# Optimization experiments

Measured on AMD Instinct MI355X. Metric: run time of the kernel, lower is better.

## Reference

```python
import jax, jax.numpy as jnp
import numpy as np

NUM_HEADS = 4
NUM_GROUPS = 32
EPS = 1e-5


def setup_inputs() -> dict:
    key = jax.random.key(0)
    ks = jax.random.split(key, 4)
    ch = 256
    x = jax.random.normal(ks[0], (16, ch, 32, 32), dtype=jnp.float32)
    gn_w = jnp.ones((ch,), jnp.float32)
    gn_b = jnp.zeros((ch,), jnp.float32)
    # conv1x1 weights, kaiming-ish scale
    qkv_w = jax.random.normal(ks[1], (3 * ch, ch), dtype=jnp.float32) / np.sqrt(ch)
    qkv_b = jnp.zeros((3 * ch,), jnp.float32)
    proj_w = jax.random.normal(ks[2], (ch, ch), dtype=jnp.float32) / np.sqrt(ch)
    proj_b = jnp.zeros((ch,), jnp.float32)
    return {"x": x, "gn_w": gn_w, "gn_b": gn_b, "qkv_w": qkv_w,
            "qkv_b": qkv_b, "proj_w": proj_w, "proj_b": proj_b}


def _group_norm(x, w, b):
    bsz, c, h, wd = x.shape
    g = NUM_GROUPS
    xg = x.reshape(bsz, g, c // g, h, wd)
    mean = xg.mean(axis=(2, 3, 4), keepdims=True)
    var = xg.var(axis=(2, 3, 4), keepdims=True)
    xg = (xg - mean) * jax.lax.rsqrt(var + EPS)
    return xg.reshape(bsz, c, h, wd) * w[None, :, None, None] + b[None, :, None, None]


def reference(x, gn_w, gn_b, qkv_w, qkv_b, proj_w, proj_b):
    b, c, h, w = x.shape
    hd = c // NUM_HEADS
    scale = hd ** (-0.5)
    y = _group_norm(x, gn_w, gn_b)
    # 1x1 conv == channel matmul
    qkv = jnp.einsum('oc,bchw->bohw', qkv_w, y) + qkv_b[None, :, None, None]
    q, k, v = jnp.split(qkv, 3, axis=1)
    q = q.reshape(b, NUM_HEADS, hd, h * w)
    k = k.reshape(b, NUM_HEADS, hd, h * w)
    v = v.reshape(b, NUM_HEADS, hd, h * w)
    attn = jnp.einsum('bhdi,bhdj->bhij', q * scale, k)
    attn = jax.nn.softmax(attn, axis=-1)
    out = jnp.einsum('bhij,bhdj->bhdi', attn, v)
    out = out.reshape(b, c, h, w)
    out = jnp.einsum('oc,bchw->bohw', proj_w, out) + proj_b[None, :, None, None]
    return x + out
```

## Files before the change

### kernel.cpp

```cpp
#include <hip/hip_runtime.h>
#include <cstddef>

#define B_   16
#define C_   256
#define HW_  1024
#define NH_  4
#define NG_  32
#define CPG_ 8

typedef __attribute__((ext_vector_type(8))) short bf16x8;
typedef __attribute__((ext_vector_type(8))) _Float16 f16x8;
typedef __attribute__((ext_vector_type(4))) float f32x4;

#define MFMA16B(a, b, c) __builtin_amdgcn_mfma_f32_16x16x32_bf16(a, b, c, 0, 0, 0)
#define MFMA16H(a, b, c) __builtin_amdgcn_mfma_f32_16x16x32_f16(a, b, c, 0, 0, 0)

__device__ __forceinline__ float bf2f(unsigned short h) {
    unsigned int u = ((unsigned int)h) << 16;
    return __builtin_bit_cast(float, u);
}
__device__ __forceinline__ unsigned short f2bf(float f) {
    unsigned int u = __builtin_bit_cast(unsigned int, f);
    u += 0x7FFFu + ((u >> 16) & 1u);
    return (unsigned short)(u >> 16);
}
__device__ __forceinline__ unsigned packbf(float a, float b) {
    unsigned ua = __builtin_bit_cast(unsigned, a) + 0x8000u;
    unsigned ub = __builtin_bit_cast(unsigned, b) + 0x8000u;
    return __builtin_amdgcn_perm(ub, ua, 0x07060302u);
}
__device__ __forceinline__ unsigned pkh(float a, float b) {
    auto h2 = __builtin_amdgcn_cvt_pkrtz(a, b);
    return __builtin_bit_cast(unsigned, h2);
}

__global__ __launch_bounds__(256) void wcvt_kernel(
    const float* __restrict__ qw, const float* __restrict__ pw,
    unsigned short* __restrict__ oq, unsigned short* __restrict__ op)
{
    int i = blockIdx.x * 256 + threadIdx.x;
    const float* s; unsigned short* d; int j;
    if (i < 49152) { s = qw; d = oq; j = i; }
    else           { s = pw; d = op; j = i - 49152; }
    float4 f = ((const float4*)s)[j];
    uint2 u = {pkh(f.x, f.y), pkh(f.z, f.w)};
    *(uint2*)&d[(size_t)j * 4] = u;
}

__global__ __launch_bounds__(256) void gn_kernel(
    const float* __restrict__ x,
    const float* __restrict__ gw,
    const float* __restrict__ gb,
    float2* __restrict__ scsh)
{
    int blk = blockIdx.x;
    const float* xg = x + (size_t)blk * CPG_ * HW_;
    const int N = CPG_ * HW_;

    float s = 0.f, ss = 0.f;
    for (int e = threadIdx.x * 4; e < N; e += 1024) {
        float4 v4 = *(const float4*)&xg[e];
        s  += v4.x + v4.y + v4.z + v4.w;
        ss += v4.x * v4.x + v4.y * v4.y + v4.z * v4.z + v4.w * v4.w;
    }
    #pragma unroll
    for (int off = 32; off > 0; off >>= 1) {
        s  += __shfl_down(s, off, 64);
        ss += __shfl_down(ss, off, 64);
    }
    __shared__ float red[8];
    __shared__ float2 stf;
    int lane = threadIdx.x & 63, wv = threadIdx.x >> 6;
    if (lane == 0) { red[wv] = s; red[4 + wv] = ss; }
    __syncthreads();
    if (threadIdx.x == 0) {
        float S  = red[0] + red[1] + red[2] + red[3];
        float SS = red[4] + red[5] + red[6] + red[7];
        float mean = S / (float)N;
        float var  = SS / (float)N - mean * mean;
        stf = make_float2(mean, rsqrtf(var + 1e-5f));
    }
    __syncthreads();
    if (threadIdx.x < 8) {
        int ch = (blk & 31) * CPG_ + threadIdx.x;
        float sc = stf.y * gw[ch];
        float sh = gb[ch] - stf.x * sc;
        scsh[blk * 8 + threadIdx.x] = make_float2(sc, sh);
    }
}

template <bool FUSE_GN, bool FINAL>
__global__ __launch_bounds__(256) void gemm_mfma_kernel(
    const unsigned short* __restrict__ W16,
    const float* __restrict__ Xf,
    const unsigned short* __restrict__ Xh,
    const float* __restrict__ bias,
    const float2* __restrict__ scsh,
    const float* __restrict__ res,
    float* __restrict__ outF,
    unsigned short* __restrict__ qT,
    unsigned short* __restrict__ kT,
    unsigned short* __restrict__ vN,
    int M, int K, int N)
{
    __shared__ union {
        struct { unsigned short A[2][128][40]; unsigned short Bt[2][64][40]; } st;
        unsigned short nd[2][64][72];
        unsigned short mn[128][72];
    } L;

    const int b  = blockIdx.z;
    const int m0 = blockIdx.y * 128, n0 = blockIdx.x * 64;
    const int t  = threadIdx.x;
    const int l15 = t & 15, quad = (t >> 4) & 3;
    const int wave = t >> 6, wm = wave >> 1, wn = wave & 1;

    union HF { uint4 q; f16x8 v; };

    f32x4 acc[4][2];
    #pragma unroll
    for (int mt = 0; mt < 4; ++mt)
        #pragma unroll
        for (int nt = 0; nt < 2; ++nt)
            acc[mt][nt] = (f32x4){0.f, 0.f, 0.f, 0.f};

    const int ar = t >> 1, akh = (t & 1) * 16;
    const int bn = t & 63, bkb = t >> 6;

    uint4 pa0, pa1;
    float pv[8];
    unsigned short ph[8];
    float2 ss[8];

    auto PREF = [&](int k0) {
        const unsigned short* wp = &W16[(size_t)(m0 + ar) * K + k0 + akh];
        pa0 = *(const uint4*)wp;
        pa1 = *(const uint4*)(wp + 8);
        int ch = k0 + bkb * 8;
        if (FINAL) {
            const unsigned short* xp = &Xh[((size_t)b * K + ch) * N + n0 + bn];
            #pragma unroll
            for (int j = 0; j < 8; ++j) ph[j] = xp[(size_t)j * N];
        } else {
            const float* xp = &Xf[((size_t)b * K + ch) * N + n0 + bn];
            #pragma unroll
            for (int j = 0; j < 8; ++j) pv[j] = xp[(size_t)j * N];
            if (FUSE_GN) {
                const float4* sp = (const float4*)&scsh[b * C_ + ch];
                #pragma unroll
                for (int q2 = 0; q2 < 4; ++q2) ((float4*)ss)[q2] = sp[q2];
            }
        }
    };

    PREF(0);
    const int NIT = K / 32;
    for (int it = 0; it < NIT; ++it) {
        const int bsel = it & 1;
        *(uint4*)&L.st.A[bsel][ar][akh]     = pa0;
        *(uint4*)&L.st.A[bsel][ar][akh + 8] = pa1;
        {
            float v[8];
            if (FINAL) {
                #pragma unroll
                for (int j = 0; j < 8; ++j) v[j] = bf2f(ph[j]);
            } else {
                #pragma unroll
                for (int j = 0; j < 8; ++j) v[j] = pv[j];
                if (FUSE_GN) {
                    #pragma unroll
                    for (int j = 0; j < 8; ++j) v[j] = v[j] * ss[j].x + ss[j].y;
                }
            }
            uint4 bw = {pkh(v[0], v[1]), pkh(v[2], v[3]), pkh(v[4], v[5]), pkh(v[6], v[7])};
            *(uint4*)&L.st.Bt[bsel][bn][bkb * 8] = bw;
        }
        __syncthreads();
        if (it + 1 < NIT) PREF((it + 1) * 32);
        HF af[4], bfv[2];
        #pragma unroll
        for (int mt = 0; mt < 4; ++mt)
            af[mt].q = *(const uint4*)&L.st.A[bsel][wm * 64 + mt * 16 + l15][quad * 8];
        #pragma unroll
        for (int nt = 0; nt < 2; ++nt)
            bfv[nt].q = *(const uint4*)&L.st.Bt[bsel][wn * 32 + nt * 16 + l15][quad * 8];
        #pragma unroll
        for (int mt = 0; mt < 4; ++mt)
            #pragma unroll
            for (int nt = 0; nt < 2; ++nt)
                acc[mt][nt] = MFMA16H(af[mt].v, bfv[nt].v, acc[mt][nt]);
    }
    __syncthreads();

    if (FINAL) {
        #pragma unroll
        for (int mt = 0; mt < 4; ++mt) {
            #pragma unroll
            for (int rr = 0; rr < 4; ++rr) {
                int m = m0 + wm * 64 + mt * 16 + quad * 4 + rr;
                float bv = bias[m];
                #pragma unroll
                for (int nt = 0; nt < 2; ++nt) {
                    int n = n0 + wn * 32 + nt * 16 + l15;
                    size_t off = ((size_t)b * M + m) * (size_t)N + n;
                    outF[off] = acc[mt][nt][rr] + bv + res[off];
                }
            }
        }
    } else if (m0 < 512) {
        #pragma unroll
        for (int mt = 0; mt < 4; ++mt)
            #pragma unroll
            for (int rr = 0; rr < 4; ++rr) {
                int dl = mt * 16 + quad * 4 + rr;
                float bv = bias[m0 + wm * 64 + dl];
                #pragma unroll
                for (int nt = 0; nt < 2; ++nt)
                    L.nd[wm][wn * 32 + nt * 16 + l15][dl] = f2bf(acc[mt][nt][rr] + bv);
            }
        __syncthreads();
        unsigned short* dst = (m0 < 256) ? qT : kT;
        int headbase = (m0 & 255) >> 6;
        int hl = t >> 7, tt = t & 127;
        int nl = tt >> 1, db = (tt & 1) * 32;
        const unsigned short* src = &L.nd[hl][nl][db];
        unsigned short* gp = &dst[(((size_t)(b * 4 + headbase + hl)) * 1024 + n0 + nl) * 64 + db];
        uint4 u0 = *(const uint4*)(src);
        uint4 u1 = *(const uint4*)(src + 8);
        uint4 u2 = *(const uint4*)(src + 16);
        uint4 u3 = *(const uint4*)(src + 24);
        *(uint4*)(gp)      = u0;
        *(uint4*)(gp + 8)  = u1;
        *(uint4*)(gp + 16) = u2;
        *(uint4*)(gp + 24) = u3;
    } else {
        #pragma unroll
        for (int mt = 0; mt < 4; ++mt)
            #pragma unroll
            for (int rr = 0; rr < 4; ++rr) {
                int ml = wm * 64 + mt * 16 + quad * 4 + rr;
                float bv = bias[m0 + ml];
                #pragma unroll
                for (int nt = 0; nt < 2; ++nt)
                    L.mn[ml][wn * 32 + nt * 16 + l15] = f2bf(acc[mt][nt][rr] + bv);
            }
        __syncthreads();
        int ml = t & 127, nb = t >> 7;
        const unsigned short* src = &L.mn[ml][nb * 32];
        unsigned short* gp = &vN[((size_t)b * 256 + (m0 - 512) + ml) * 1024 + n0 + nb * 32];
        uint4 u0 = *(const uint4*)(src);
        uint4 u1 = *(const uint4*)(src + 8);
        uint4 u2 = *(const uint4*)(src + 16);
        uint4 u3 = *(const uint4*)(src + 24);
        *(uint4*)(gp)      = u0;
        *(uint4*)(gp + 8)  = u1;
        *(uint4*)(gp + 16) = u2;
        *(uint4*)(gp + 24) = u3;
    }
}

__global__ __launch_bounds__(256) void attn_mfma_kernel(
    const unsigned short* __restrict__ qT,
    const unsigned short* __restrict__ kT,
    const unsigned short* __restrict__ vN,
    unsigned short* __restrict__ att)
{
    __shared__ unsigned short Kt[2][64][68];
    __shared__ unsigned short Vs[2][64][68];

    const int t    = threadIdx.x;
    const int wv   = t >> 6;
    const int l15  = t & 15;
    const int quad = (t >> 4) & 3;
    const int bh   = blockIdx.x;
    const int i0   = blockIdx.y * 64;
    const float cs = 0.125f * 1.44269504f;

    union FragU { uint4 q; uint2 u2[2]; unsigned u[4]; bf16x8 v; };

    FragU qf[2];
    {
        const unsigned short* qg = qT + (size_t)bh * (1024 * 64);
        int qrow = i0 + wv * 16 + l15;
        #pragma unroll
        for (int kt = 0; kt < 2; ++kt)
            qf[kt].q = *(const uint4*)&qg[(size_t)qrow * 64 + kt * 32 + quad * 8];
    }

    f32x4 accO[4];
    #pragma unroll
    for (int m = 0; m < 4; ++m) accO[m] = (f32x4){0.f, 0.f, 0.f, 0.f};
    float l_i = 0.f;

    const unsigned short* kg = kT + (size_t)bh * (1024 * 64);
    const unsigned short* vg = vN + (size_t)bh * (64 * 1024);

    const int slbase = l15 + ((quad & 1) << 5);
    const bool upper = (t & 32) != 0;
    const int sr = t >> 4, sc = (t & 15) * 4;

    ushort4 kr[4], vr[4];
    #pragma unroll
    for (int p = 0; p < 4; ++p) {
        int rr = sr + p * 16;
        kr[p] = *(const ushort4*)&kg[(size_t)rr * 64 + sc];
        vr[p] = *(const ushort4*)&vg[(size_t)rr * 1024 + sc];
    }

    for (int it = 0; it < 16; ++it) {
        const int bsel = it & 1;
        #pragma unroll
        for (int p = 0; p < 4; ++p) {
            int rr = sr + p * 16;
            *(ushort4*)&Kt[bsel][rr][sc] = kr[p];
            *(ushort4*)&Vs[bsel][rr][sc] = vr[p];
        }
        __syncthreads();
        if (it < 15) {
            int j0n = (it + 1) * 64;
            #pragma unroll
            for (int p = 0; p < 4; ++p) {
                int rr = sr + p * 16;
                kr[p] = *(const ushort4*)&kg[(size_t)(j0n + rr) * 64 + sc];
                vr[p] = *(const ushort4*)&vg[(size_t)rr * 1024 + j0n + sc];
            }
        }

        f32x4 accS[4];
        #pragma unroll
        for (int mt = 0; mt < 4; ++mt) {
            FragU ak[2];
            #pragma unroll
            for (int kt = 0; kt < 2; ++kt) {
                const unsigned short* p = &Kt[bsel][mt * 16 + l15][kt * 32 + quad * 8];
                ak[kt].u2[0] = *(const uint2*)p;
                ak[kt].u2[1] = *(const uint2*)(p + 4);
            }
            f32x4 z = (f32x4){0.f, 0.f, 0.f, 0.f};
            z = MFMA16B(ak[0].v, qf[0].v, z);
            z = MFMA16B(ak[1].v, qf[1].v, z);
            accS[mt] = z;
        }

        float rs = 0.f;
        unsigned pk[4][2];
        #pragma unroll
        for (int mt = 0; mt < 4; ++mt) {
            float p0 = exp2f(cs * accS[mt][0]);
            float p1 = exp2f(cs * accS[mt][1]);
            float p2 = exp2f(cs * accS[mt][2]);
            float p3 = exp2f(cs * accS[mt][3]);
            rs += (p0 + p1) + (p2 + p3);
            pk[mt][0] = packbf(p0, p1);
            pk[mt][1] = packbf(p2, p3);
        }
        rs += __shfl_xor(rs, 16, 64);
        rs += __shfl_xor(rs, 32, 64);
        l_i += rs;

        FragU bfr[2];
        #pragma unroll
        for (int kt = 0; kt < 2; ++kt)
            #pragma unroll
            for (int w4 = 0; w4 < 4; ++w4) {
                int sl = slbase + ((w4 >> 1) << 4);
                int lo = __shfl((int)pk[2 * kt + 0][w4 & 1], sl, 64);
                int hi = __shfl((int)pk[2 * kt + 1][w4 & 1], sl, 64);
                bfr[kt].u[w4] = (unsigned)(upper ? hi : lo);
            }

        #pragma unroll
        for (int mtd = 0; mtd < 4; ++mtd) {
            FragU av[2];
            #pragma unroll
            for (int kt = 0; kt < 2; ++kt) {
                const unsigned short* p = &Vs[bsel][mtd * 16 + l15][kt * 32 + quad * 8];
                av[kt].u2[0] = *(const uint2*)p;
                av[kt].u2[1] = *(const uint2*)(p + 4);
            }
            accO[mtd] = MFMA16B(av[0].v, bfr[0].v, accO[mtd]);
            accO[mtd] = MFMA16B(av[1].v, bfr[1].v, accO[mtd]);
        }
    }

    float inv = 1.f / l_i;
    unsigned short* ob = att + (size_t)bh * (64 * 1024) + i0 + wv * 16;
    #pragma unroll
    for (int mtd = 0; mtd < 4; ++mtd)
        #pragma unroll
        for (int rr = 0; rr < 4; ++rr) {
            int d = mtd * 16 + quad * 4 + rr;
            ob[(size_t)d * 1024 + l15] = f2bf(accO[mtd][rr] * inv);
        }
}

extern "C" void kernel_launch(void* const* d_in, const int* in_sizes, int n_in,
                              void* d_out, int out_size, void* d_ws, size_t ws_size,
                              hipStream_t stream)
{
    const float* x      = (const float*)d_in[0];
    const float* gn_w   = (const float*)d_in[1];
    const float* gn_b   = (const float*)d_in[2];
    const float* qkv_w  = (const float*)d_in[3];
    const float* qkv_b  = (const float*)d_in[4];
    const float* proj_w = (const float*)d_in[5];
    const float* proj_b = (const float*)d_in[6];
    float* out = (float*)d_out;

    char* ws = (char*)d_ws;
    float2* scsh = (float2*)ws;
    unsigned short* w16q = (unsigned short*)(ws + 32768);
    unsigned short* w16p = w16q + 768 * 256;
    unsigned short* qT   = w16p + 256 * 256;
    unsigned short* kT   = qT + (size_t)B_ * NH_ * HW_ * 64;
    unsigned short* vN   = kT + (size_t)B_ * NH_ * HW_ * 64;
    unsigned short* att  = vN + (size_t)B_ * C_ * HW_;
    (void)in_sizes; (void)n_in; (void)out_size; (void)ws_size;

    wcvt_kernel<<<dim3(256), 256, 0, stream>>>(qkv_w, proj_w, w16q, w16p);
    gn_kernel<<<dim3(B_ * NG_), 256, 0, stream>>>(x, gn_w, gn_b, scsh);

    gemm_mfma_kernel<true, false><<<dim3(HW_ / 64, (3 * C_) / 128, B_), 256, 0, stream>>>(
        w16q, x, nullptr, qkv_b, scsh, nullptr, nullptr,
        qT, kT, vN, 3 * C_, C_, HW_);

    attn_mfma_kernel<<<dim3(NH_ * B_, HW_ / 64), 256, 0, stream>>>(qT, kT, vN, att);

    gemm_mfma_kernel<false, true><<<dim3(HW_ / 64, C_ / 128, B_), 256, 0, stream>>>(
        w16p, nullptr, att, proj_b, nullptr, x, out,
        nullptr, nullptr, nullptr, C_, C_, HW_);
}
```

Measured before the change: 161.2 us.

## Split attention over key halves with a combine kernel and fold softmax scale into Q

Splits the key dimension of the attention kernel into two halves (split-K style, grid z=2), writing unnormalized partial outputs and row sums to workspace, then adds a separate combine kernel that sums the partials and normalizes. The softmax scale times log2(e) is folded into the Q projection epilogue. The attention kernel also drops register-prefetch double buffering in favor of single-buffered 16-byte loads with padded LDS rows, and sets an occupancy hint. Together these aim to raise parallelism and occupancy, at the cost of extra partial-output traffic, an extra launch, and bf16 rounding of the partial sums.

```diff
diff --git a/kernel.cpp b/kernel.cpp
--- a/kernel.cpp
+++ b/kernel.cpp
@@ -7,6 +7,7 @@
 #define NH_  4
 #define NG_  32
 #define CPG_ 8
+#define CS_  0.18033688f
 
 typedef __attribute__((ext_vector_type(8))) short bf16x8;
 typedef __attribute__((ext_vector_type(8))) _Float16 f16x8;
@@ -208,6 +209,7 @@
             }
         }
     } else if (m0 < 512) {
+        const float qsc = (m0 < 256) ? CS_ : 1.f;
         #pragma unroll
         for (int mt = 0; mt < 4; ++mt)
             #pragma unroll
@@ -216,7 +218,7 @@
                 float bv = bias[m0 + wm * 64 + dl];
                 #pragma unroll
                 for (int nt = 0; nt < 2; ++nt)
-                    L.nd[wm][wn * 32 + nt * 16 + l15][dl] = f2bf(acc[mt][nt][rr] + bv);
+                    L.nd[wm][wn * 32 + nt * 16 + l15][dl] = f2bf((acc[mt][nt][rr] + bv) * qsc);
             }
         __syncthreads();
         unsigned short* dst = (m0 < 256) ? qT : kT;
@@ -259,14 +261,15 @@
     }
 }
 
-__global__ __launch_bounds__(256) void attn_mfma_kernel(
+__global__ __launch_bounds__(256, 8) void attn_mfma_kernel(
     const unsigned short* __restrict__ qT,
     const unsigned short* __restrict__ kT,
     const unsigned short* __restrict__ vN,
-    unsigned short* __restrict__ att)
-{
-    __shared__ unsigned short Kt[2][64][68];
-    __shared__ unsigned short Vs[2][64][68];
+    unsigned short* __restrict__ OP,
+    float* __restrict__ LP)
+{
+    __shared__ unsigned short Kt[64][72];
+    __shared__ unsigned short Vs[64][72];
 
     const int t    = threadIdx.x;
     const int wv   = t >> 6;
@@ -274,9 +277,9 @@
     const int quad = (t >> 4) & 3;
     const int bh   = blockIdx.x;
     const int i0   = blockIdx.y * 64;
-    const float cs = 0.125f * 1.44269504f;
-
-    union FragU { uint4 q; uint2 u2[2]; unsigned u[4]; bf16x8 v; };
+    const int jh   = blockIdx.z;
+
+    union FragU { uint4 q; unsigned u[4]; bf16x8 v; };
 
     FragU qf[2];
     {
@@ -297,45 +300,31 @@
 
     const int slbase = l15 + ((quad & 1) << 5);
     const bool upper = (t & 32) != 0;
-    const int sr = t >> 4, sc = (t & 15) * 4;
-
-    ushort4 kr[4], vr[4];
-    #pragma unroll
-    for (int p = 0; p < 4; ++p) {
-        int rr = sr + p * 16;
-        kr[p] = *(const ushort4*)&kg[(size_t)rr * 64 + sc];
-        vr[p] = *(const ushort4*)&vg[(size_t)rr * 1024 + sc];
-    }
-
-    for (int it = 0; it < 16; ++it) {
-        const int bsel = it & 1;
-        #pragma unroll
-        for (int p = 0; p < 4; ++p) {
-            int rr = sr + p * 16;
-            *(ushort4*)&Kt[bsel][rr][sc] = kr[p];
-            *(ushort4*)&Vs[bsel][rr][sc] = vr[p];
+    const int sr = t >> 2, sc = (t & 3) * 16;
+
+    for (int it = 0; it < 8; ++it) {
+        const int j0 = (jh * 8 + it) * 64;
+        {
+            const unsigned short* kp = &kg[(size_t)(j0 + sr) * 64 + sc];
+            const unsigned short* vp = &vg[(size_t)sr * 1024 + j0 + sc];
+            uint4 k0 = *(const uint4*)kp;
+            uint4 k1 = *(const uint4*)(kp + 8);
+            uint4 v0 = *(const uint4*)vp;
+            uint4 v1 = *(const uint4*)(vp + 8);
+            *(uint4*)&Kt[sr][sc]     = k0;
+            *(uint4*)&Kt[sr][sc + 8] = k1;
+            *(uint4*)&Vs[sr][sc]     = v0;
+            *(uint4*)&Vs[sr][sc + 8] = v1;
         }
         __syncthreads();
-        if (it < 15) {
-            int j0n = (it + 1) * 64;
-            #pragma unroll
-            for (int p = 0; p < 4; ++p) {
-                int rr = sr + p * 16;
-                kr[p] = *(const ushort4*)&kg[(size_t)(j0n + rr) * 64 + sc];
-                vr[p] = *(const ushort4*)&vg[(size_t)rr * 1024 + j0n + sc];
-            }
-        }
 
         f32x4 accS[4];
         #pragma unroll
         for (int mt = 0; mt < 4; ++mt) {
             FragU ak[2];
             #pragma unroll
-            for (int kt = 0; kt < 2; ++kt) {
-                const unsigned short* p = &Kt[bsel][mt * 16 + l15][kt * 32 + quad * 8];
-                ak[kt].u2[0] = *(const uint2*)p;
-                ak[kt].u2[1] = *(const uint2*)(p + 4);
-            }
+            for (int kt = 0; kt < 2; ++kt)
+                ak[kt].q = *(const uint4*)&Kt[mt * 16 + l15][kt * 32 + quad * 8];
             f32x4 z = (f32x4){0.f, 0.f, 0.f, 0.f};
             z = MFMA16B(ak[0].v, qf[0].v, z);
             z = MFMA16B(ak[1].v, qf[1].v, z);
@@ -346,10 +335,10 @@
         unsigned pk[4][2];
         #pragma unroll
         for (int mt = 0; mt < 4; ++mt) {
-            float p0 = exp2f(cs * accS[mt][0]);
-            float p1 = exp2f(cs * accS[mt][1]);
-            float p2 = exp2f(cs * accS[mt][2]);
-            float p3 = exp2f(cs * accS[mt][3]);
+            float p0 = exp2f(accS[mt][0]);
+            float p1 = exp2f(accS[mt][1]);
+            float p2 = exp2f(accS[mt][2]);
+            float p3 = exp2f(accS[mt][3]);
             rs += (p0 + p1) + (p2 + p3);
             pk[mt][0] = packbf(p0, p1);
             pk[mt][1] = packbf(p2, p3);
@@ -373,25 +362,44 @@
         for (int mtd = 0; mtd < 4; ++mtd) {
             FragU av[2];
             #pragma unroll
-            for (int kt = 0; kt < 2; ++kt) {
-                const unsigned short* p = &Vs[bsel][mtd * 16 + l15][kt * 32 + quad * 8];
-                av[kt].u2[0] = *(const uint2*)p;
-                av[kt].u2[1] = *(const uint2*)(p + 4);
-            }
+            for (int kt = 0; kt < 2; ++kt)
+                av[kt].q = *(const uint4*)&Vs[mtd * 16 + l15][kt * 32 + quad * 8];
             accO[mtd] = MFMA16B(av[0].v, bfr[0].v, accO[mtd]);
             accO[mtd] = MFMA16B(av[1].v, bfr[1].v, accO[mtd]);
         }
-    }
-
-    float inv = 1.f / l_i;
-    unsigned short* ob = att + (size_t)bh * (64 * 1024) + i0 + wv * 16;
+        __syncthreads();
+    }
+
+    unsigned short* ob = OP + ((size_t)jh * 64 + bh) * (64 * 1024) + i0 + wv * 16;
     #pragma unroll
     for (int mtd = 0; mtd < 4; ++mtd)
         #pragma unroll
         for (int rr = 0; rr < 4; ++rr) {
             int d = mtd * 16 + quad * 4 + rr;
-            ob[(size_t)d * 1024 + l15] = f2bf(accO[mtd][rr] * inv);
-        }
+            ob[(size_t)d * 1024 + l15] = f2bf(accO[mtd][rr]);
+        }
+    if (quad == 0)
+        LP[((size_t)jh * 64 + bh) * 1024 + i0 + wv * 16 + l15] = l_i;
+}
+
+__global__ __launch_bounds__(256) void attn_combine_kernel(
+    const unsigned short* __restrict__ OP,
+    const float* __restrict__ LP,
+    unsigned short* __restrict__ att)
+{
+    size_t e0 = ((size_t)blockIdx.x * 256 + threadIdx.x) * 4;
+    int bh  = (int)(e0 >> 16);
+    int col = (int)(e0 & 1023);
+    ushort4 a = *(const ushort4*)&OP[e0];
+    ushort4 b = *(const ushort4*)&OP[(size_t)(1 << 22) + e0];
+    float4 la = *(const float4*)&LP[(size_t)bh * 1024 + col];
+    float4 lb = *(const float4*)&LP[(size_t)(1 << 16) + (size_t)bh * 1024 + col];
+    ushort4 o;
+    o.x = f2bf((bf2f(a.x) + bf2f(b.x)) / (la.x + lb.x));
+    o.y = f2bf((bf2f(a.y) + bf2f(b.y)) / (la.y + lb.y));
+    o.z = f2bf((bf2f(a.z) + bf2f(b.z)) / (la.z + lb.z));
+    o.w = f2bf((bf2f(a.w) + bf2f(b.w)) / (la.w + lb.w));
+    *(ushort4*)&att[e0] = o;
 }
 
 extern "C" void kernel_launch(void* const* d_in, const int* in_sizes, int n_in,
@@ -415,6 +423,8 @@
     unsigned short* kT   = qT + (size_t)B_ * NH_ * HW_ * 64;
     unsigned short* vN   = kT + (size_t)B_ * NH_ * HW_ * 64;
     unsigned short* att  = vN + (size_t)B_ * C_ * HW_;
+    unsigned short* OP   = att + (size_t)B_ * C_ * HW_;
+    float*          LP   = (float*)(OP + (size_t)2 * B_ * C_ * HW_);
     (void)in_sizes; (void)n_in; (void)out_size; (void)ws_size;
 
     wcvt_kernel<<<dim3(256), 256, 0, stream>>>(qkv_w, proj_w, w16q, w16p);
@@ -424,7 +434,8 @@
         w16q, x, nullptr, qkv_b, scsh, nullptr, nullptr,
         qT, kT, vN, 3 * C_, C_, HW_);
 
-    attn_mfma_kernel<<<dim3(NH_ * B_, HW_ / 64), 256, 0, stream>>>(qT, kT, vN, att);
+    attn_mfma_kernel<<<dim3(NH_ * B_, HW_ / 64, 2), 256, 0, stream>>>(qT, kT, vN, OP, LP);
+    attn_combine_kernel<<<dim3(8192), 256, 0, stream>>>(OP, LP, att);
 
     gemm_mfma_kernel<false, true><<<dim3(HW_ / 64, C_ / 128, B_), 256, 0, stream>>>(
         w16p, nullptr, att, proj_b, nullptr, x, out,
```

Result: slower. 241.0 us (+49.5%).
